# Kernel tuning notes

Hardware: AMD Instinct MI355X
Metric: run time of the kernel (lower is better)

Reference implementation:

```python
import jax, jax.numpy as jnp
import numpy as np

B, S, H = 1024, 64, 256  # batch, seq_length (num_for_predict), hidden_size (= in_channels)


def setup_inputs() -> dict:
    key = jax.random.key(0)
    ks = jax.random.split(key, 7)
    std_h = np.sqrt(2.0 / H).astype(np.float32)  # He init of hidden state, as in initHidden
    std_w = np.sqrt(1.0 / H).astype(np.float32)
    return {
        "x": jax.random.normal(ks[0], (B, S, H), dtype=jnp.float32),
        "h0": jax.random.normal(ks[1], (B, H), dtype=jnp.float32) * std_h,
        "c0": jax.random.normal(ks[2], (B, H), dtype=jnp.float32) * std_h,
        "W_ih": jax.random.normal(ks[3], (4 * H, H), dtype=jnp.float32) * std_w,
        "W_hh": jax.random.normal(ks[4], (4 * H, H), dtype=jnp.float32) * std_w,
        "b_ih": jnp.zeros((4 * H,), dtype=jnp.float32),
        "b_hh": jnp.zeros((4 * H,), dtype=jnp.float32),
        "seq_length": S,
    }


def reference(x, h0, c0, W_ih, W_hh, b_ih, b_hh, seq_length):
    # x: [B, T, D] with D == H (in_channels forced to hidden_size). RNN_layer == 1.
    Hd = h0.shape[-1]
    xs = jnp.swapaxes(x[:, :seq_length, :], 0, 1)  # [S, B, D]
    # precompute input projections for all steps (same math, fewer tiny GEMMs)
    x_gates = jnp.einsum("sbd,gd->sbg", xs, W_ih) + b_ih  # [S, B, 4H]

    def step(carry, xg):
        h, c = carry
        gates = xg + h @ W_hh.T + b_hh  # [B, 4H]
        i, f, g, o = jnp.split(gates, 4, axis=-1)
        c_new = jax.nn.sigmoid(f) * c + jax.nn.sigmoid(i) * jnp.tanh(g)
        h_new = jax.nn.sigmoid(o) * jnp.tanh(c_new)
        return (h_new, c_new), h_new

    (_, _), hs = jax.lax.scan(step, (h0, c0), x_gates)  # hs: [S, B, H]
    outputs = jnp.swapaxes(hs, 0, 1)  # [B, S, H]
    hiddens = outputs[:, None, :, :]  # [B, RNN_layer=1, S, H]
    return outputs, hiddens
```

## Files before the change

### kernel.cpp

```cpp
#include <hip/hip_runtime.h>


typedef __attribute__((ext_vector_type(8))) short short8;
typedef __attribute__((ext_vector_type(4))) float f32x4;
typedef unsigned long long u64;
typedef unsigned int u32;
typedef unsigned short u16;

#define B_ 1024
#define S_ 64
#define H_ 256
#define G_ 1024
#define KW 512
#define OUTN (B_*S_*H_)
#define APITCH 520
#define GPITCH 132
#define NCL 32
#define CWG 8
#define B128 (B_*128)

__device__ __forceinline__ u16 f2bf(float f){
    u32 u = __builtin_bit_cast(u32, f);
    u = (u + 0x7fffu + ((u >> 16) & 1u)) >> 16;
    return (u16)u;
}
__device__ __forceinline__ float sigm(float v){ return 1.0f/(1.0f + __expf(-v)); }
__device__ __forceinline__ float tanh_(float v){ return 2.0f/(1.0f + __expf(-2.0f*v)) - 1.0f; }

__device__ __forceinline__ void wg_barrier_lds(){
    asm volatile("s_waitcnt lgkmcnt(0)" ::: "memory");
    __builtin_amdgcn_sched_barrier(0);
    __builtin_amdgcn_s_barrier();
    __builtin_amdgcn_sched_barrier(0);
}

__global__ __launch_bounds__(256) void prep_kernel(const float* __restrict__ Wih,
        const float* __restrict__ Whh, const float* __restrict__ bih,
        const float* __restrict__ bhh, const float* __restrict__ h0,
        u16* __restrict__ Wc, float* __restrict__ bias, u64* __restrict__ hq){
    int idx = blockIdx.x*256 + threadIdx.x;
    if (idx < G_*KW){
        int g = idx >> 9, k = idx & 511;
        float v = (k < H_) ? Wih[g*H_ + k] : Whh[g*H_ + (k - H_)];
        Wc[idx] = f2bf(v);
    }
    if (idx < G_) bias[idx] = bih[idx] + bhh[idx];
    if (idx < B128){
        int b = idx >> 7, c = idx & 127;
        u32 hp = (u32)f2bf(h0[b*H_ + 2*c]) | ((u32)f2bf(h0[b*H_ + 2*c + 1]) << 16);
        hq[idx] = (u64)hp;
        hq[B128 + idx] = 0xFFFFFFFF00000000ull;
    }
}

__global__ __launch_bounds__(512, 2) void lstm_kernel(
        const float* __restrict__ x, const float* __restrict__ c0,
        const u16* __restrict__ Wc, const float* __restrict__ bias,
        u64* hq, float* __restrict__ out){
    __shared__ u16 At[32*APITCH];
    __shared__ float Gt[32*GPITCH];

    const int tid  = threadIdx.x;
    const int lane = tid & 63;
    const int w    = tid >> 6;
    const int wn   = w >> 1, tn = w & 1;
    const int nl   = lane & 15, kg = lane >> 4;
    const int bid  = blockIdx.x;
    const int cl   = bid & (NCL-1);
    const int j    = bid >> 5;
    const int b0   = cl * 32;
    const int d0   = j * 32;

    const int grow_idx = wn*256 + d0 + tn*16 + nl;
    short8 wf[16];
    {
        const u16* wp = Wc + (size_t)grow_idx*KW + kg*8;
        #pragma unroll
        for (int kf = 0; kf < 16; ++kf) wf[kf] = *(const short8*)(wp + kf*32);
    }
    #pragma unroll
    for (int kf = 0; kf < 16; ++kf) asm volatile("" : "+v"(wf[kf]));
    const float bias_l = bias[grow_idx];

    const int sb = tid >> 4;
    const int dp = tid & 15;
    float c0r, c1r;
    {
        float2 cv = *(const float2*)(c0 + (size_t)(b0+sb)*H_ + d0 + 2*dp);
        c0r = cv.x; c1r = cv.y;
    }

    int rc[7];
    #pragma unroll
    for (int i = 0; i < 7; ++i){
        int m = i*16 + dp;
        rc[i] = m + (m >= 16*j ? 16 : 0);
    }

    float xr[16];
    {
        const float* xp = x + ((size_t)(b0+sb)*S_ + 0)*H_ + dp*16;
        #pragma unroll
        for (int q = 0; q < 4; ++q){
            f32x4 v = *(const f32x4*)(xp + q*4);
            xr[q*4+0]=v[0]; xr[q*4+1]=v[1]; xr[q*4+2]=v[2]; xr[q*4+3]=v[3];
        }
        u16 tmp[16];
        #pragma unroll
        for (int q = 0; q < 16; ++q) tmp[q] = f2bf(xr[q]);
        *(short8*)(At + sb*APITCH + dp*16)     = *(const short8*)tmp;
        *(short8*)(At + sb*APITCH + dp*16 + 8) = *(const short8*)(tmp+8);
    }
    {
        const u64* hb = hq + (size_t)(b0+sb)*128;
        #pragma unroll
        for (int i = 0; i < 8; ++i){
            int c = dp + 16*i;
            u64 v = hb[c];
            *(u32*)(At + sb*APITCH + H_ + 2*c) = (u32)v;
        }
    }
    {
        const float* xp = x + ((size_t)(b0+sb)*S_ + 1)*H_ + dp*16;
        #pragma unroll
        for (int q = 0; q < 4; ++q){
            f32x4 v = *(const f32x4*)(xp + q*4);
            xr[q*4+0]=v[0]; xr[q*4+1]=v[1]; xr[q*4+2]=v[2]; xr[q*4+3]=v[3];
        }
    }
    __syncthreads();

    u64 gv[7];

    #pragma unroll 1
    for (int s = 0; s < S_; ++s){
        f32x4 acc0 = (f32x4){bias_l, bias_l, bias_l, bias_l};
        f32x4 acc1 = acc0;
        const u16* ar = At + nl*APITCH + kg*8;
        #pragma unroll
        for (int kf = 0; kf < 8; ++kf){
            short8 a0 = *(const short8*)(ar + kf*32);
            short8 a1 = *(const short8*)(ar + 16*APITCH + kf*32);
            acc0 = __builtin_amdgcn_mfma_f32_16x16x32_bf16(a0, wf[kf], acc0, 0, 0, 0);
            acc1 = __builtin_amdgcn_mfma_f32_16x16x32_bf16(a1, wf[kf], acc1, 0, 0, 0);
        }

        if (s > 0){
            const u64* gb = hq + (size_t)(s & 1)*B128 + (size_t)(b0+sb)*128;
            const u32 want = (u32)s;
            int guard = 0;
            for (;;){
                bool ok = true;
                #pragma unroll
                for (int i = 0; i < 7; ++i)
                    if ((u32)(gv[i] >> 32) != want) ok = false;
                if (__all((int)ok)) break;
                if (++guard > (1<<16)) break;
                #pragma unroll
                for (int i = 0; i < 7; ++i)
                    if ((u32)(gv[i] >> 32) != want)
                        gv[i] = __hip_atomic_load(gb + rc[i], __ATOMIC_RELAXED,
                                                  __HIP_MEMORY_SCOPE_AGENT);
            }
            #pragma unroll
            for (int i = 0; i < 7; ++i)
                *(u32*)(At + sb*APITCH + H_ + 2*rc[i]) = (u32)gv[i];
        }
        wg_barrier_lds();

        #pragma unroll
        for (int kf = 8; kf < 16; ++kf){
            short8 a0 = *(const short8*)(ar + kf*32);
            short8 a1 = *(const short8*)(ar + 16*APITCH + kf*32);
            acc0 = __builtin_amdgcn_mfma_f32_16x16x32_bf16(a0, wf[kf], acc0, 0, 0, 0);
            acc1 = __builtin_amdgcn_mfma_f32_16x16x32_bf16(a1, wf[kf], acc1, 0, 0, 0);
        }

        if (s + 1 < S_){
            u16 tmp[16];
            #pragma unroll
            for (int q = 0; q < 16; ++q) tmp[q] = f2bf(xr[q]);
            *(short8*)(At + sb*APITCH + dp*16)     = *(const short8*)tmp;
            *(short8*)(At + sb*APITCH + dp*16 + 8) = *(const short8*)(tmp+8);
        }
        {
            const int colc = wn*32 + tn*16 + nl;
            #pragma unroll
            for (int jj = 0; jj < 4; ++jj){
                Gt[(kg*4 + jj)*GPITCH + colc]      = acc0[jj];
                Gt[(16 + kg*4 + jj)*GPITCH + colc] = acc1[jj];
            }
        }
        wg_barrier_lds();

        {
            const float* gr = Gt + sb*GPITCH + 2*dp;
            float iv0 = gr[0],  iv1 = gr[1];
            float fv0 = gr[32], fv1 = gr[33];
            float gv0 = gr[64], gv1 = gr[65];
            float ov0 = gr[96], ov1 = gr[97];
            float cn0 = sigm(fv0)*c0r + sigm(iv0)*tanh_(gv0);
            float cn1 = sigm(fv1)*c1r + sigm(iv1)*tanh_(gv1);
            float hn0 = sigm(ov0)*tanh_(cn0);
            float hn1 = sigm(ov1)*tanh_(cn1);
            c0r = cn0; c1r = cn1;

            if (s < S_-1){
                u32 hpk = (u32)f2bf(hn0) | ((u32)f2bf(hn1) << 16);
                u64 pv  = ((u64)(u32)(s+1) << 32) | (u64)hpk;
                __hip_atomic_store(hq + (size_t)((s+1)&1)*B128
                                   + (size_t)(b0+sb)*128 + (d0>>1) + dp, pv,
                                   __ATOMIC_RELAXED, __HIP_MEMORY_SCOPE_AGENT);
                *(u32*)(At + sb*APITCH + H_ + d0 + 2*dp) = hpk;
            }
            size_t o = ((size_t)(b0+sb)*S_ + s)*H_ + d0 + 2*dp;
            float2 hv; hv.x = hn0; hv.y = hn1;
            *(float2*)(out + o) = hv;
            *(float2*)(out + OUTN + o) = hv;
        }
        if (s + 2 < S_){
            const float* xp = x + ((size_t)(b0+sb)*S_ + (s+2))*H_ + dp*16;
            #pragma unroll
            for (int q = 0; q < 4; ++q){
                f32x4 v = *(const f32x4*)(xp + q*4);
                xr[q*4+0]=v[0]; xr[q*4+1]=v[1]; xr[q*4+2]=v[2]; xr[q*4+3]=v[3];
            }
        }
        if (s + 1 < S_){
            const u64* gb = hq + (size_t)((s+1)&1)*B128 + (size_t)(b0+sb)*128;
            #pragma unroll
            for (int i = 0; i < 7; ++i)
                gv[i] = __hip_atomic_load(gb + rc[i], __ATOMIC_RELAXED,
                                          __HIP_MEMORY_SCOPE_AGENT);
        }
    }
}

extern "C" void kernel_launch(void* const* d_in, const int* in_sizes, int n_in,
                              void* d_out, int out_size, void* d_ws, size_t ws_size,
                              hipStream_t stream){
    const float* x   = (const float*)d_in[0];
    const float* h0  = (const float*)d_in[1];
    const float* c0  = (const float*)d_in[2];
    const float* Wih = (const float*)d_in[3];
    const float* Whh = (const float*)d_in[4];
    const float* bih = (const float*)d_in[5];
    const float* bhh = (const float*)d_in[6];

    u16*   Wc   = (u16*)d_ws;
    float* bias = (float*)((char*)d_ws + 0x100000);
    u64*   hq   = (u64*)((char*)d_ws + 0x110000);
    float* outp = (float*)d_out;

    prep_kernel<<<(G_*KW + 255)/256, 256, 0, stream>>>(Wih, Whh, bih, bhh, h0, Wc, bias, hq);

    void* args[] = {(void*)&x, (void*)&c0, (void*)&Wc, (void*)&bias,
                    (void*)&hq, (void*)&outp};
    hipLaunchCooperativeKernel((void*)lstm_kernel, dim3(NCL*CWG), dim3(512), args, 0, stream);
}
```

Measured before the change: 217.9 us.

## Use per-half-word step tags and sc0 L2 loads/stores for h exchange with slow-path fallback

Each exchanged h value now carries its step tag in the high 16 bits of each 32-bit half, so a 64-bit word is self-validating even if the two halves become visible separately. Stores and polls on a fast buffer use inline global_load/store_dwordx2 with sc0 instead of agent-scope atomics. A mirrored buffer written with atomic stores serves as a fallback after 48 failed polls. The aim is to cut the latency of cross-workgroup hidden-state synchronisation, at the cost of an extra store per step, more packing and unpacking work, and reliance on cache-coherence behaviour of sc0 accesses.

Result: slower. 281.4 us (+29.1%).

```diff
diff --git a/kernel.cpp b/kernel.cpp
--- a/kernel.cpp
+++ b/kernel.cpp
@@ -27,6 +27,16 @@
 __device__ __forceinline__ float sigm(float v){ return 1.0f/(1.0f + __expf(-v)); }
 __device__ __forceinline__ float tanh_(float v){ return 2.0f/(1.0f + __expf(-2.0f*v)) - 1.0f; }
 
+__device__ __forceinline__ void st_l2_x2(u64* p, u64 v){
+    asm volatile("global_store_dwordx2 %0, %1, off sc0" :: "v"(p), "v"(v) : "memory");
+}
+__device__ __forceinline__ void ld_l2_x2(u64* dst, const u64* p){
+    asm volatile("global_load_dwordx2 %0, %1, off sc0" : "=v"(*dst) : "v"(p) : "memory");
+}
+__device__ __forceinline__ void wait_vm0(){
+    asm volatile("s_waitcnt vmcnt(0)" ::: "memory");
+    __builtin_amdgcn_sched_barrier(0);
+}
 __device__ __forceinline__ void wg_barrier_lds(){
     asm volatile("s_waitcnt lgkmcnt(0)" ::: "memory");
     __builtin_amdgcn_sched_barrier(0);
@@ -37,7 +47,8 @@
 __global__ __launch_bounds__(256) void prep_kernel(const float* __restrict__ Wih,
         const float* __restrict__ Whh, const float* __restrict__ bih,
         const float* __restrict__ bhh, const float* __restrict__ h0,
-        u16* __restrict__ Wc, float* __restrict__ bias, u64* __restrict__ hq){
+        u16* __restrict__ Wc, float* __restrict__ bias,
+        u64* __restrict__ hqf, u64* __restrict__ hqs){
     int idx = blockIdx.x*256 + threadIdx.x;
     if (idx < G_*KW){
         int g = idx >> 9, k = idx & 511;
@@ -47,16 +58,19 @@
     if (idx < G_) bias[idx] = bih[idx] + bhh[idx];
     if (idx < B128){
         int b = idx >> 7, c = idx & 127;
-        u32 hp = (u32)f2bf(h0[b*H_ + 2*c]) | ((u32)f2bf(h0[b*H_ + 2*c + 1]) << 16);
-        hq[idx] = (u64)hp;
-        hq[B128 + idx] = 0xFFFFFFFF00000000ull;
+        u32 plo = (u32)f2bf(h0[b*H_ + 2*c]);
+        u32 phi = (u32)f2bf(h0[b*H_ + 2*c + 1]);
+        u64 v = ((u64)phi << 32) | plo;
+        hqf[idx] = v;                hqs[idx] = v;
+        hqf[B128 + idx] = 0xFFFF0000FFFF0000ull;
+        hqs[B128 + idx] = 0xFFFF0000FFFF0000ull;
     }
 }
 
 __global__ __launch_bounds__(512, 2) void lstm_kernel(
         const float* __restrict__ x, const float* __restrict__ c0,
         const u16* __restrict__ Wc, const float* __restrict__ bias,
-        u64* hq, float* __restrict__ out){
+        u64* hqf, u64* hqs, float* __restrict__ out){
     __shared__ u16 At[32*APITCH];
     __shared__ float Gt[32*GPITCH];
 
@@ -112,12 +126,13 @@
         *(short8*)(At + sb*APITCH + dp*16 + 8) = *(const short8*)(tmp+8);
     }
     {
-        const u64* hb = hq + (size_t)(b0+sb)*128;
+        const u64* hb = hqf + (size_t)(b0+sb)*128;
         #pragma unroll
         for (int i = 0; i < 8; ++i){
             int c = dp + 16*i;
             u64 v = hb[c];
-            *(u32*)(At + sb*APITCH + H_ + 2*c) = (u32)v;
+            u32 lo = (u32)v, hi = (u32)(v >> 32);
+            *(u32*)(At + sb*APITCH + H_ + 2*c) = (lo & 0xFFFFu) | (hi << 16);
         }
     }
     {
@@ -130,7 +145,8 @@
     }
     __syncthreads();
 
-    u64 gv[7];
+    u64 gv[7] = {};
+    bool slowmode = false;
 
     #pragma unroll 1
     for (int s = 0; s < S_; ++s){
@@ -146,25 +162,37 @@
         }
 
         if (s > 0){
-            const u64* gb = hq + (size_t)(s & 1)*B128 + (size_t)(b0+sb)*128;
             const u32 want = (u32)s;
+            const u64* gfb = hqf + (size_t)(s & 1)*B128 + (size_t)(b0+sb)*128;
+            const u64* gsb = hqs + (size_t)(s & 1)*B128 + (size_t)(b0+sb)*128;
+            wait_vm0();
             int guard = 0;
             for (;;){
                 bool ok = true;
                 #pragma unroll
-                for (int i = 0; i < 7; ++i)
-                    if ((u32)(gv[i] >> 32) != want) ok = false;
+                for (int i = 0; i < 7; ++i){
+                    u32 lo = (u32)gv[i], hi = (u32)(gv[i] >> 32);
+                    ok = ok && ((lo >> 16) == want) && ((hi >> 16) == want);
+                }
                 if (__all((int)ok)) break;
-                if (++guard > (1<<16)) break;
-                #pragma unroll
-                for (int i = 0; i < 7; ++i)
-                    if ((u32)(gv[i] >> 32) != want)
-                        gv[i] = __hip_atomic_load(gb + rc[i], __ATOMIC_RELAXED,
+                if (++guard > (1<<13)) break;
+                if (guard >= 48) slowmode = true;
+                if (!slowmode){
+                    #pragma unroll
+                    for (int i = 0; i < 7; ++i) ld_l2_x2(&gv[i], gfb + rc[i]);
+                    wait_vm0();
+                } else {
+                    #pragma unroll
+                    for (int i = 0; i < 7; ++i)
+                        gv[i] = __hip_atomic_load(gsb + rc[i], __ATOMIC_RELAXED,
                                                   __HIP_MEMORY_SCOPE_AGENT);
-            }
-            #pragma unroll
-            for (int i = 0; i < 7; ++i)
-                *(u32*)(At + sb*APITCH + H_ + 2*rc[i]) = (u32)gv[i];
+                }
+            }
+            #pragma unroll
+            for (int i = 0; i < 7; ++i){
+                u32 lo = (u32)gv[i], hi = (u32)(gv[i] >> 32);
+                *(u32*)(At + sb*APITCH + H_ + 2*rc[i]) = (lo & 0xFFFFu) | (hi << 16);
+            }
         }
         wg_barrier_lds();
 
@@ -206,11 +234,15 @@
             c0r = cn0; c1r = cn1;
 
             if (s < S_-1){
+                u32 t16 = (u32)(s+1) << 16;
+                u32 plo = t16 | (u32)f2bf(hn0);
+                u32 phi = t16 | (u32)f2bf(hn1);
+                u64 pv  = ((u64)phi << 32) | plo;
+                size_t slot = (size_t)((s+1)&1)*B128 + (size_t)(b0+sb)*128 + (d0>>1) + dp;
+                st_l2_x2(hqf + slot, pv);
+                __hip_atomic_store(hqs + slot, pv,
+                                   __ATOMIC_RELAXED, __HIP_MEMORY_SCOPE_AGENT);
                 u32 hpk = (u32)f2bf(hn0) | ((u32)f2bf(hn1) << 16);
-                u64 pv  = ((u64)(u32)(s+1) << 32) | (u64)hpk;
-                __hip_atomic_store(hq + (size_t)((s+1)&1)*B128
-                                   + (size_t)(b0+sb)*128 + (d0>>1) + dp, pv,
-                                   __ATOMIC_RELAXED, __HIP_MEMORY_SCOPE_AGENT);
                 *(u32*)(At + sb*APITCH + H_ + d0 + 2*dp) = hpk;
             }
             size_t o = ((size_t)(b0+sb)*S_ + s)*H_ + d0 + 2*dp;
@@ -218,6 +250,11 @@
             *(float2*)(out + o) = hv;
             *(float2*)(out + OUTN + o) = hv;
         }
+        if (s + 1 < S_){
+            const u64* gfb = hqf + (size_t)((s+1)&1)*B128 + (size_t)(b0+sb)*128;
+            #pragma unroll
+            for (int i = 0; i < 7; ++i) ld_l2_x2(&gv[i], gfb + rc[i]);
+        }
         if (s + 2 < S_){
             const float* xp = x + ((size_t)(b0+sb)*S_ + (s+2))*H_ + dp*16;
             #pragma unroll
@@ -225,13 +262,6 @@
                 f32x4 v = *(const f32x4*)(xp + q*4);
                 xr[q*4+0]=v[0]; xr[q*4+1]=v[1]; xr[q*4+2]=v[2]; xr[q*4+3]=v[3];
             }
-        }
-        if (s + 1 < S_){
-            const u64* gb = hq + (size_t)((s+1)&1)*B128 + (size_t)(b0+sb)*128;
-            #pragma unroll
-            for (int i = 0; i < 7; ++i)
-                gv[i] = __hip_atomic_load(gb + rc[i], __ATOMIC_RELAXED,
-                                          __HIP_MEMORY_SCOPE_AGENT);
         }
     }
 }
@@ -249,12 +279,14 @@
 
     u16*   Wc   = (u16*)d_ws;
     float* bias = (float*)((char*)d_ws + 0x100000);
-    u64*   hq   = (u64*)((char*)d_ws + 0x110000);
+    u64*   hqf  = (u64*)((char*)d_ws + 0x110000);
+    u64*   hqs  = (u64*)((char*)d_ws + 0x310000);
     float* outp = (float*)d_out;
 
-    prep_kernel<<<(G_*KW + 255)/256, 256, 0, stream>>>(Wih, Whh, bih, bhh, h0, Wc, bias, hq);
+    prep_kernel<<<(G_*KW + 255)/256, 256, 0, stream>>>(Wih, Whh, bih, bhh, h0,
+                                                       Wc, bias, hqf, hqs);
 
     void* args[] = {(void*)&x, (void*)&c0, (void*)&Wc, (void*)&bias,
-                    (void*)&hq, (void*)&outp};
+                    (void*)&hqf, (void*)&hqs, (void*)&outp};
     hipLaunchCooperativeKernel((void*)lstm_kernel, dim3(NCL*CWG), dim3(512), args, 0, stream);
 }
```
